# Optimization experiments

Hardware: AMD Instinct MI355X
Metric: run time of the kernel (lower is better)

## Reference

```python
import jax, jax.numpy as jnp
import numpy as np

VOL_SHAPE = (256, 256, 256)
DELTA = 1
EPS = 1e-8


def _radius_bins(shape, delta):
    # Frequency-index radius map (equivalent to distance from DC with fft wraparound),
    # binned into shells of width `delta`. Computed once with numpy (constant).
    axes = [np.fft.fftfreq(n) * n for n in shape]
    grids = np.meshgrid(*axes, indexing='ij')
    r = np.sqrt(sum(g.astype(np.float64) ** 2 for g in grids))
    bins = np.floor(r / delta).astype(np.int32)
    return bins.ravel(), int(bins.max()) + 1

_BINS, _NUM_SHELLS = _radius_bins(VOL_SHAPE, DELTA)
_BINS_J = jnp.asarray(_BINS)


def setup_inputs() -> dict:
    key = jax.random.key(0)
    kx, ky = jax.random.split(key)
    shp = (2, 1) + VOL_SHAPE
    X = jax.random.normal(kx, shp, dtype=jnp.float32)
    Y = jax.random.normal(ky, shp, dtype=jnp.float32)
    return {"X": X, "Y": Y}


def _fsc(X, Y):
    B, C = X.shape[0], X.shape[1]
    Fx = jnp.fft.fftn(X, axes=(-3, -2, -1))  # complex64 [B,C,D,H,W]
    Fy = jnp.fft.fftn(Y, axes=(-3, -2, -1))
    N = VOL_SHAPE[0] * VOL_SHAPE[1] * VOL_SHAPE[2]
    # Per-voxel quantities, flattened over the volume: [B*C, N]
    num = (Fx.real * Fy.real + Fx.imag * Fy.imag).reshape(B * C, N)  # Re(Fx * conj(Fy))
    px = (Fx.real ** 2 + Fx.imag ** 2).reshape(B * C, N)
    py = (Fy.real ** 2 + Fy.imag ** 2).reshape(B * C, N)
    seg = lambda v: jax.ops.segment_sum(v, _BINS_J, num_segments=_NUM_SHELLS)
    num_s = jax.vmap(seg)(num)  # [B*C, S]
    px_s = jax.vmap(seg)(px)
    py_s = jax.vmap(seg)(py)
    fsc = num_s / jnp.sqrt(px_s * py_s + EPS)  # [B*C, S]
    return fsc.reshape(B, C, _NUM_SHELLS)


def reference(X, Y):
    fsc = _fsc(X, Y)
    # size_average=True: average over radii, channel and batch -> scalar
    return jnp.mean(fsc)
```

## Files before the change

kernel.cpp:

```cpp
#include <hip/hip_runtime.h>
#include <math.h>

#define VOL (256 * 256 * 256)
#define NSHELL 222
#define SBINS 224
#define PI_D 3.14159265358979323846
#define VSTRIDE ((size_t)129 << 16)

__device__ __forceinline__ int rev4(int e) {
  return ((e & 3) << 6) | (((e >> 2) & 3) << 4) | (((e >> 4) & 3) << 2) | ((e >> 6) & 3);
}

__global__ void tw_init(float2* __restrict__ gtw) {
  int t = threadIdx.x;
  double a = -2.0 * PI_D * (double)t / 256.0;
  gtw[t] = make_float2((float)cos(a), (float)sin(a));
}

__device__ __forceinline__ void bfly4_dif(float* re, float* im, const float* twr,
                                          const float* twi, int a0, int a1, int a2,
                                          int a3, int t1, int t2, int t3) {
  float x0r = re[a0], x0i = im[a0], x1r = re[a1], x1i = im[a1];
  float x2r = re[a2], x2i = im[a2], x3r = re[a3], x3i = im[a3];
  float s02r = x0r + x2r, s02i = x0i + x2i, d02r = x0r - x2r, d02i = x0i - x2i;
  float s13r = x1r + x3r, s13i = x1i + x3i, d13r = x1r - x3r, d13i = x1i - x3i;
  re[a0] = s02r + s13r; im[a0] = s02i + s13i;
  float c1r = d02r + d13i, c1i = d02i - d13r;
  re[a1] = c1r * twr[t1] - c1i * twi[t1]; im[a1] = c1r * twi[t1] + c1i * twr[t1];
  float c2r = s02r - s13r, c2i = s02i - s13i;
  re[a2] = c2r * twr[t2] - c2i * twi[t2]; im[a2] = c2r * twi[t2] + c2i * twr[t2];
  float c3r = d02r - d13i, c3i = d02i + d13r;
  re[a3] = c3r * twr[t3] - c3i * twi[t3]; im[a3] = c3r * twi[t3] + c3i * twr[t3];
}

__device__ __forceinline__ void seg_flush(float* sh, int sb, float nv, float pv,
                                          float qv, int l) {
#pragma unroll
  for (int d = 1; d < 64; d <<= 1) {
    int sbo = __shfl_down(sb, d);
    float no = __shfl_down(nv, d);
    float po = __shfl_down(pv, d);
    float qo = __shfl_down(qv, d);
    if (l + d < 64 && sbo == sb) { nv += no; pv += po; qv += qo; }
  }
  int sbp = __shfl_up(sb, 1);
  if (l == 0 || sbp != sb) {
    atomicAdd(&sh[3 * sb + 0], nv);
    atomicAdd(&sh[3 * sb + 1], pv);
    atomicAdd(&sh[3 * sb + 2], qv);
  }
}

__global__ __launch_bounds__(256) void fft_z_pack(const float* __restrict__ X,
                                                  const float* __restrict__ Y,
                                                  float2* __restrict__ Gx,
                                                  float2* __restrict__ Gy,
                                                  const float2* __restrict__ gtw) {
  __shared__ float zr[256 * 17], zi[256 * 17];
  __shared__ float twr[256], twi[256];
  int t = threadIdx.x;
  { float2 w = gtw[t]; twr[t] = w.x; twi[t] = w.y; }
  int li = t >> 4, c = t & 15;
  int y = blockIdx.x >> 4;
  int x0 = (blockIdx.x & 15) << 4;
  const float4* xp = (const float4*)(X + (((size_t)(x0 + li)) << 16) + ((size_t)y << 8));
  const float4* yp = (const float4*)(Y + (((size_t)(x0 + li)) << 16) + ((size_t)y << 8));
#pragma unroll
  for (int it = 0; it < 4; ++it) {
    int e4 = c + 16 * it;
    float4 a = xp[e4];
    float4 b = yp[e4];
    int e = e4 << 2;
    zr[(e + 0) * 17 + li] = a.x; zi[(e + 0) * 17 + li] = b.x;
    zr[(e + 1) * 17 + li] = a.y; zi[(e + 1) * 17 + li] = b.y;
    zr[(e + 2) * 17 + li] = a.z; zi[(e + 2) * 17 + li] = b.z;
    zr[(e + 3) * 17 + li] = a.w; zi[(e + 3) * 17 + li] = b.w;
  }
  __syncthreads();
#pragma unroll
  for (int s = 0; s < 4; ++s) {
    int M = 64 >> (2 * s);
    int F = 1 << (2 * s);
#pragma unroll
    for (int ib = 0; ib < 4; ++ib) {
      int j = c + 16 * ib;
      int p = j & (M - 1);
      int jb = j >> (6 - 2 * s);
      int base = jb * (M << 2) + p;
      bfly4_dif(zr, zi, twr, twi, base * 17 + li, (base + M) * 17 + li,
                (base + 2 * M) * 17 + li, (base + 3 * M) * 17 + li,
                (p * F) & 255, (2 * p * F) & 255, (3 * p * F) & 255);
    }
    __syncthreads();
  }
  int krow = t >> 4, xi = t & 15;
#pragma unroll
  for (int g = 0; g < 9; ++g) {
    int kz = g * 16 + krow;
    if (kz <= 128) {
      int s1 = rev4(kz & 255);
      int s2 = rev4((256 - kz) & 255);
      float ar = zr[s1 * 17 + xi], ai = zi[s1 * 17 + xi];
      float br = zr[s2 * 17 + xi], bi = zi[s2 * 17 + xi];
      size_t off = ((size_t)kz << 16) + ((size_t)y << 8) + (size_t)(x0 + xi);
      Gx[off] = make_float2(0.5f * (ar + br), 0.5f * (ai - bi));
      Gy[off] = make_float2(0.5f * (ai + bi), 0.5f * (br - ar));
    }
  }
}

__global__ __launch_bounds__(256) void fft_y(float2* __restrict__ G,
                                             const float2* __restrict__ gtw) {
  __shared__ float sr[256 * 17], si[256 * 17];
  __shared__ float twr[256], twi[256];
  int t = threadIdx.x;
  { float2 w = gtw[t]; twr[t] = w.x; twi[t] = w.y; }
  int xi = t & 15, c = t >> 4;
  int x0 = blockIdx.x << 4;
  int kz = blockIdx.y;
  float2* Gp = G + (size_t)blockIdx.z * VSTRIDE + ((size_t)kz << 16) + (size_t)(x0 + xi);
#pragma unroll
  for (int i = 0; i < 16; ++i) {
    int e = c * 16 + i;
    float2 v = Gp[(size_t)e << 8];
    sr[e * 17 + xi] = v.x;
    si[e * 17 + xi] = v.y;
  }
  __syncthreads();
#pragma unroll
  for (int s = 0; s < 4; ++s) {
    int M = 64 >> (2 * s);
    int F = 1 << (2 * s);
#pragma unroll
    for (int ib = 0; ib < 4; ++ib) {
      int j = c + 16 * ib;
      int p = j & (M - 1);
      int jb = j >> (6 - 2 * s);
      int base = jb * (M << 2) + p;
      bfly4_dif(sr, si, twr, twi, base * 17 + xi, (base + M) * 17 + xi,
                (base + 2 * M) * 17 + xi, (base + 3 * M) * 17 + xi,
                (p * F) & 255, (2 * p * F) & 255, (3 * p * F) & 255);
    }
    __syncthreads();
  }
#pragma unroll
  for (int i = 0; i < 16; ++i) {
    int e = c * 16 + i;
    Gp[(size_t)e << 8] = make_float2(sr[e * 17 + xi], si[e * 17 + xi]);
  }
}

__global__ __launch_bounds__(512) void fft_x_reduce(const float2* __restrict__ G,
                                                    double* __restrict__ sums,
                                                    const float2* __restrict__ gtw) {
  __shared__ float Axr[256 * 9], Axi[256 * 9], Ayr[256 * 9], Ayi[256 * 9];
  __shared__ float twr[256], twi[256];
  __shared__ float sh[3 * SBINS];
  int t = threadIdx.x;
  if (t < 256) { float2 w = gtw[t]; twr[t] = w.x; twi[t] = w.y; }
  for (int i = t; i < 3 * SBINS; i += 512) sh[i] = 0.f;
  int vol = t >> 8, tt = t & 255;
  int li = tt >> 5, c = tt & 31;
  int kz = blockIdx.y;
  int r0 = blockIdx.x << 3;
  const float2* Gp = G + (size_t)vol * VSTRIDE + ((size_t)kz << 16) + ((size_t)(r0 + li) << 8);
  float* pr = vol ? Ayr : Axr;
  float* pi = vol ? Ayi : Axi;
#pragma unroll
  for (int it = 0; it < 8; ++it) {
    int e = c + 32 * it;
    float2 v = Gp[e];
    pr[e * 9 + li] = v.x;
    pi[e * 9 + li] = v.y;
  }
  __syncthreads();
#pragma unroll
  for (int s = 0; s < 3; ++s) {
    int M = 64 >> (2 * s);
    int F = 1 << (2 * s);
#pragma unroll
    for (int ib = 0; ib < 2; ++ib) {
      int j = c + 32 * ib;
      int p = j & (M - 1);
      int jb = j >> (6 - 2 * s);
      int base = jb * (M << 2) + p;
      bfly4_dif(pr, pi, twr, twi, base * 9 + li, (base + M) * 9 + li,
                (base + 2 * M) * 9 + li, (base + 3 * M) * 9 + li,
                (p * F) & 255, (2 * p * F) & 255, (3 * p * F) & 255);
    }
    __syncthreads();
  }
  float or_[2][4], oi_[2][4];
#pragma unroll
  for (int ib = 0; ib < 2; ++ib) {
    int j = c + 32 * ib;
    int base = 4 * j;
    float x0r = pr[(base + 0) * 9 + li], x0i = pi[(base + 0) * 9 + li];
    float x1r = pr[(base + 1) * 9 + li], x1i = pi[(base + 1) * 9 + li];
    float x2r = pr[(base + 2) * 9 + li], x2i = pi[(base + 2) * 9 + li];
    float x3r = pr[(base + 3) * 9 + li], x3i = pi[(base + 3) * 9 + li];
    float s02r = x0r + x2r, s02i = x0i + x2i, d02r = x0r - x2r, d02i = x0i - x2i;
    float s13r = x1r + x3r, s13i = x1i + x3i, d13r = x1r - x3r, d13i = x1i - x3i;
    or_[ib][0] = s02r + s13r; oi_[ib][0] = s02i + s13i;
    or_[ib][1] = d02r + d13i; oi_[ib][1] = d02i - d13r;
    or_[ib][2] = s02r - s13r; oi_[ib][2] = s02i - s13i;
    or_[ib][3] = d02r - d13i; oi_[ib][3] = d02i + d13r;
  }
  __syncthreads();
#pragma unroll
  for (int ib = 0; ib < 2; ++ib) {
    int j = c + 32 * ib;
#pragma unroll
    for (int q = 0; q < 4; ++q) {
      int slot = (q << 6) | ((j & 3) << 4) | (((j >> 2) & 3) << 2) | (j >> 4);
      pr[slot * 9 + li] = or_[ib][q];
      pi[slot * 9 + li] = oi_[ib][q];
    }
  }
  __syncthreads();
  int fz = kz - ((kz & 128) ? 256 : 0);
  int fz2 = fz * fz;
  {
    int w = t >> 6, l = t & 63;
    int ky = rev4(r0 + w);
    int fy = ky - ((ky & 128) ? 256 : 0);
    int c2 = fy * fy + fz2;
#pragma unroll
    for (int pass = 0; pass < 2; ++pass) {
      int kx = pass * 64 + l;
      int a = kx * 9 + w;
      float xr = Axr[a], xi = Axi[a], yr = Ayr[a], yi = Ayi[a];
      float nv = xr * yr + xi * yi;
      float pv = xr * xr + xi * xi;
      float qv = yr * yr + yi * yi;
      if (kx != 0) {
        int ma = ((256 - kx) & 255) * 9 + w;
        float mxr = Axr[ma], mxi = Axi[ma], myr = Ayr[ma], myi = Ayi[ma];
        nv += mxr * myr + mxi * myi;
        pv += mxr * mxr + mxi * mxi;
        qv += myr * myr + myi * myi;
      }
      int m = kx * kx + c2;
      int sb = (int)sqrtf((float)m);
      while (sb * sb > m) --sb;
      while ((sb + 1) * (sb + 1) <= m) ++sb;
      seg_flush(sh, sb, nv, pv, qv, l);
    }
    if (l == 0) {
      int a = 128 * 9 + w;
      float xr = Axr[a], xi = Axi[a], yr = Ayr[a], yi = Ayi[a];
      int m = 16384 + c2;
      int sb = (int)sqrtf((float)m);
      while (sb * sb > m) --sb;
      while ((sb + 1) * (sb + 1) <= m) ++sb;
      atomicAdd(&sh[3 * sb + 0], xr * yr + xi * yi);
      atomicAdd(&sh[3 * sb + 1], xr * xr + xi * xi);
      atomicAdd(&sh[3 * sb + 2], yr * yr + yi * yi);
    }
  }
  __syncthreads();
  float wf = (kz == 0 || kz == 128) ? 1.f : 2.f;
  for (int i = t; i < 3 * SBINS; i += 512) {
    float vv = sh[i];
    if (vv != 0.f) atomicAdd(&sums[i], (double)(wf * vv));
  }
}

__global__ void finalize(const double* __restrict__ sums, float* __restrict__ out) {
  if (threadIdx.x == 0 && blockIdx.x == 0) {
    double acc = 0.0;
    for (int b = 0; b < 2; ++b) {
      const double* s = sums + b * 3 * SBINS;
      for (int k = 0; k < NSHELL; ++k)
        acc += s[3 * k] / sqrt(s[3 * k + 1] * s[3 * k + 2] + 1e-8);
    }
    out[0] = (float)(acc / (2.0 * (double)NSHELL));
  }
}

extern "C" void kernel_launch(void* const* d_in, const int* in_sizes, int n_in,
                              void* d_out, int out_size, void* d_ws, size_t ws_size,
                              hipStream_t stream) {
  const float* X = (const float*)d_in[0];
  const float* Y = (const float*)d_in[1];
  float2* Gx = (float2*)d_ws;
  float2* Gy = Gx + VSTRIDE;
  double* sums = (double*)((char*)d_ws + (size_t)2 * VSTRIDE * sizeof(float2));
  float2* gtw = (float2*)(sums + 2 * 3 * SBINS);

  hipMemsetAsync(sums, 0, 2 * 3 * SBINS * sizeof(double), stream);
  tw_init<<<1, 256, 0, stream>>>(gtw);

  for (int b = 0; b < 2; ++b) {
    fft_z_pack<<<4096, 256, 0, stream>>>(X + (size_t)b * VOL, Y + (size_t)b * VOL, Gx, Gy, gtw);
    fft_y<<<dim3(16, 129, 2), 256, 0, stream>>>(Gx, gtw);
    fft_x_reduce<<<dim3(32, 129), 512, 0, stream>>>(Gx, sums + b * 3 * SBINS, gtw);
  }
  finalize<<<1, 1, 0, stream>>>(sums, (float*)d_out);
}
```

Measured before the change: 715.6 us.

## Use register-resident 16x16 FFTs for y/x passes and split global atomic accumulators

Replaces the shared-memory radix-4 stage loops in the y and x FFT kernels with a register-based 16x16 decomposition. Each thread does a 16-point FFT in registers, applies twiddles, makes one shared transpose, then does a second 16-point FFT. This cuts shared-memory traffic and barriers, and the x kernel now runs with 256 threads and natural output ordering. Global double atomics are spread across 16 partial-sum copies that a parallel finalize reduces, which lowers atomic contention at the cost of higher register pressure.

```diff
diff --git a/kernel.cpp b/kernel.cpp
--- a/kernel.cpp
+++ b/kernel.cpp
@@ -4,6 +4,7 @@
 #define VOL (256 * 256 * 256)
 #define NSHELL 222
 #define SBINS 224
+#define NSPLIT 16
 #define PI_D 3.14159265358979323846
 #define VSTRIDE ((size_t)129 << 16)
 
@@ -51,6 +52,50 @@
   }
 }
 
+__device__ __forceinline__ float2 cmul(float2 a, float2 b) {
+  return make_float2(a.x * b.x - a.y * b.y, a.x * b.y + a.y * b.x);
+}
+
+__device__ __forceinline__ void fft16(float2* v) {
+  const float C1 = 0.92387953251128674f;
+  const float S1 = 0.38268343236508978f;
+  const float R2 = 0.70710678118654752f;
+  float2 s[16];
+#pragma unroll
+  for (int p = 0; p < 4; ++p) {
+    float2 a = v[p], b = v[p + 4], cc = v[p + 8], d = v[p + 12];
+    float2 t0 = make_float2(a.x + cc.x, a.y + cc.y);
+    float2 t2 = make_float2(a.x - cc.x, a.y - cc.y);
+    float2 t1 = make_float2(b.x + d.x, b.y + d.y);
+    float2 t3 = make_float2(b.x - d.x, b.y - d.y);
+    s[p]      = make_float2(t0.x + t1.x, t0.y + t1.y);
+    s[p + 4]  = make_float2(t2.x + t3.y, t2.y - t3.x);
+    s[p + 8]  = make_float2(t0.x - t1.x, t0.y - t1.y);
+    s[p + 12] = make_float2(t2.x - t3.y, t2.y + t3.x);
+  }
+  s[5]  = cmul(s[5],  make_float2(C1, -S1));
+  s[6]  = cmul(s[6],  make_float2(R2, -R2));
+  s[7]  = cmul(s[7],  make_float2(S1, -C1));
+  s[9]  = cmul(s[9],  make_float2(R2, -R2));
+  s[10] = cmul(s[10], make_float2(0.f, -1.f));
+  s[11] = cmul(s[11], make_float2(-R2, -R2));
+  s[13] = cmul(s[13], make_float2(S1, -C1));
+  s[14] = cmul(s[14], make_float2(-R2, -R2));
+  s[15] = cmul(s[15], make_float2(-C1, S1));
+#pragma unroll
+  for (int r = 0; r < 4; ++r) {
+    float2 u0 = s[4 * r], u1 = s[4 * r + 1], u2 = s[4 * r + 2], u3 = s[4 * r + 3];
+    float2 e0 = make_float2(u0.x + u2.x, u0.y + u2.y);
+    float2 e1 = make_float2(u0.x - u2.x, u0.y - u2.y);
+    float2 o0 = make_float2(u1.x + u3.x, u1.y + u3.y);
+    float2 o1 = make_float2(u1.x - u3.x, u1.y - u3.y);
+    v[r]      = make_float2(e0.x + o0.x, e0.y + o0.y);
+    v[4 + r]  = make_float2(e1.x + o1.y, e1.y - o1.x);
+    v[8 + r]  = make_float2(e0.x - o0.x, e0.y - o0.y);
+    v[12 + r] = make_float2(e1.x - o1.y, e1.y + o1.x);
+  }
+}
+
 __global__ __launch_bounds__(256) void fft_z_pack(const float* __restrict__ X,
                                                   const float* __restrict__ Y,
                                                   float2* __restrict__ Gx,
@@ -109,136 +154,94 @@
   }
 }
 
-__global__ __launch_bounds__(256) void fft_y(float2* __restrict__ G,
-                                             const float2* __restrict__ gtw) {
-  __shared__ float sr[256 * 17], si[256 * 17];
-  __shared__ float twr[256], twi[256];
-  int t = threadIdx.x;
-  { float2 w = gtw[t]; twr[t] = w.x; twi[t] = w.y; }
-  int xi = t & 15, c = t >> 4;
+__global__ __launch_bounds__(256, 4) void fft_y(float2* __restrict__ G,
+                                                const float2* __restrict__ gtw) {
+  __shared__ float2 scr[16 * 273];
+  int t = threadIdx.x;
+  int xi = t & 15, h = t >> 4;
   int x0 = blockIdx.x << 4;
   int kz = blockIdx.y;
   float2* Gp = G + (size_t)blockIdx.z * VSTRIDE + ((size_t)kz << 16) + (size_t)(x0 + xi);
-#pragma unroll
-  for (int i = 0; i < 16; ++i) {
-    int e = c * 16 + i;
-    float2 v = Gp[(size_t)e << 8];
-    sr[e * 17 + xi] = v.x;
-    si[e * 17 + xi] = v.y;
-  }
-  __syncthreads();
-#pragma unroll
-  for (int s = 0; s < 4; ++s) {
-    int M = 64 >> (2 * s);
-    int F = 1 << (2 * s);
-#pragma unroll
-    for (int ib = 0; ib < 4; ++ib) {
-      int j = c + 16 * ib;
-      int p = j & (M - 1);
-      int jb = j >> (6 - 2 * s);
-      int base = jb * (M << 2) + p;
-      bfly4_dif(sr, si, twr, twi, base * 17 + xi, (base + M) * 17 + xi,
-                (base + 2 * M) * 17 + xi, (base + 3 * M) * 17 + xi,
-                (p * F) & 255, (2 * p * F) & 255, (3 * p * F) & 255);
-    }
-    __syncthreads();
-  }
-#pragma unroll
-  for (int i = 0; i < 16; ++i) {
-    int e = c * 16 + i;
-    Gp[(size_t)e << 8] = make_float2(sr[e * 17 + xi], si[e * 17 + xi]);
-  }
-}
-
-__global__ __launch_bounds__(512) void fft_x_reduce(const float2* __restrict__ G,
-                                                    double* __restrict__ sums,
-                                                    const float2* __restrict__ gtw) {
-  __shared__ float Axr[256 * 9], Axi[256 * 9], Ayr[256 * 9], Ayi[256 * 9];
-  __shared__ float twr[256], twi[256];
+  float2 v[16];
+#pragma unroll
+  for (int m = 0; m < 16; ++m) v[m] = Gp[(size_t)((m << 4) | h) << 8];
+  fft16(v);
+#pragma unroll
+  for (int k1 = 1; k1 < 16; ++k1) v[k1] = cmul(v[k1], gtw[h * k1]);
+  int wb = xi * 273 + h * 17;
+#pragma unroll
+  for (int k1 = 0; k1 < 16; ++k1) scr[wb + k1] = v[k1];
+  __syncthreads();
+  float2 u[16];
+  int rb = xi * 273 + h;
+#pragma unroll
+  for (int j2 = 0; j2 < 16; ++j2) u[j2] = scr[rb + j2 * 17];
+  fft16(u);
+#pragma unroll
+  for (int k2 = 0; k2 < 16; ++k2) Gp[(size_t)((k2 << 4) | h) << 8] = u[k2];
+}
+
+__global__ __launch_bounds__(256, 4) void fft_x_reduce(const float2* __restrict__ G,
+                                                       double* __restrict__ sums,
+                                                       const float2* __restrict__ gtw) {
+  __shared__ float2 pool[4672];
   __shared__ float sh[3 * SBINS];
   int t = threadIdx.x;
-  if (t < 256) { float2 w = gtw[t]; twr[t] = w.x; twi[t] = w.y; }
-  for (int i = t; i < 3 * SBINS; i += 512) sh[i] = 0.f;
-  int vol = t >> 8, tt = t & 255;
-  int li = tt >> 5, c = tt & 31;
+  for (int i = t; i < 3 * SBINS; i += 256) sh[i] = 0.f;
+  int vol = t >> 7, tt = t & 127;
+  int g = tt >> 4, c = tt & 15;
   int kz = blockIdx.y;
   int r0 = blockIdx.x << 3;
-  const float2* Gp = G + (size_t)vol * VSTRIDE + ((size_t)kz << 16) + ((size_t)(r0 + li) << 8);
-  float* pr = vol ? Ayr : Axr;
-  float* pi = vol ? Ayi : Axi;
-#pragma unroll
-  for (int it = 0; it < 8; ++it) {
-    int e = c + 32 * it;
-    float2 v = Gp[e];
-    pr[e * 9 + li] = v.x;
-    pi[e * 9 + li] = v.y;
-  }
-  __syncthreads();
-#pragma unroll
-  for (int s = 0; s < 3; ++s) {
-    int M = 64 >> (2 * s);
-    int F = 1 << (2 * s);
-#pragma unroll
-    for (int ib = 0; ib < 2; ++ib) {
-      int j = c + 32 * ib;
-      int p = j & (M - 1);
-      int jb = j >> (6 - 2 * s);
-      int base = jb * (M << 2) + p;
-      bfly4_dif(pr, pi, twr, twi, base * 9 + li, (base + M) * 9 + li,
-                (base + 2 * M) * 9 + li, (base + 3 * M) * 9 + li,
-                (p * F) & 255, (2 * p * F) & 255, (3 * p * F) & 255);
-    }
+  const float2* Gp = G + (size_t)vol * VSTRIDE + ((size_t)kz << 16) + ((size_t)(r0 + g) << 8);
+  float2 v[16];
+#pragma unroll
+  for (int m = 0; m < 16; ++m) v[m] = Gp[(m << 4) | c];
+  fft16(v);
+#pragma unroll
+  for (int k1 = 1; k1 < 16; ++k1) v[k1] = cmul(v[k1], gtw[c * k1]);
+  {
+    int sbase = ((vol << 3) | g) * 280;
+#pragma unroll
+    for (int k1 = 0; k1 < 16; ++k1) pool[sbase + c * 17 + k1] = v[k1];
+    float2 u[16];
+#pragma unroll
+    for (int j2 = 0; j2 < 16; ++j2) u[j2] = pool[sbase + j2 * 17 + c];
+    fft16(u);
     __syncthreads();
-  }
-  float or_[2][4], oi_[2][4];
-#pragma unroll
-  for (int ib = 0; ib < 2; ++ib) {
-    int j = c + 32 * ib;
-    int base = 4 * j;
-    float x0r = pr[(base + 0) * 9 + li], x0i = pi[(base + 0) * 9 + li];
-    float x1r = pr[(base + 1) * 9 + li], x1i = pi[(base + 1) * 9 + li];
-    float x2r = pr[(base + 2) * 9 + li], x2i = pi[(base + 2) * 9 + li];
-    float x3r = pr[(base + 3) * 9 + li], x3i = pi[(base + 3) * 9 + li];
-    float s02r = x0r + x2r, s02i = x0i + x2i, d02r = x0r - x2r, d02i = x0i - x2i;
-    float s13r = x1r + x3r, s13i = x1i + x3i, d13r = x1r - x3r, d13i = x1i - x3i;
-    or_[ib][0] = s02r + s13r; oi_[ib][0] = s02i + s13i;
-    or_[ib][1] = d02r + d13i; oi_[ib][1] = d02i - d13r;
-    or_[ib][2] = s02r - s13r; oi_[ib][2] = s02i - s13i;
-    or_[ib][3] = d02r - d13i; oi_[ib][3] = d02i + d13r;
-  }
-  __syncthreads();
-#pragma unroll
-  for (int ib = 0; ib < 2; ++ib) {
-    int j = c + 32 * ib;
-#pragma unroll
-    for (int q = 0; q < 4; ++q) {
-      int slot = (q << 6) | ((j & 3) << 4) | (((j >> 2) & 3) << 2) | (j >> 4);
-      pr[slot * 9 + li] = or_[ib][q];
-      pi[slot * 9 + li] = oi_[ib][q];
+    float2* A = pool + vol * 2336;
+#pragma unroll
+    for (int k2 = 0; k2 < 16; ++k2) {
+      int kx = (k2 << 4) | c;
+      A[kx * 9 + k2 + g] = u[k2];
     }
   }
   __syncthreads();
   int fz = kz - ((kz & 128) ? 256 : 0);
   int fz2 = fz * fz;
-  {
-    int w = t >> 6, l = t & 63;
-    int ky = rev4(r0 + w);
+  int w = t >> 6, l = t & 63;
+  const float2* Ax = pool;
+  const float2* Ay = pool + 2336;
+#pragma unroll
+  for (int rr = 0; rr < 2; ++rr) {
+    int row = (w << 1) | rr;
+    int ky = r0 + row;
     int fy = ky - ((ky & 128) ? 256 : 0);
     int c2 = fy * fy + fz2;
 #pragma unroll
     for (int pass = 0; pass < 2; ++pass) {
-      int kx = pass * 64 + l;
-      int a = kx * 9 + w;
-      float xr = Axr[a], xi = Axi[a], yr = Ayr[a], yi = Ayi[a];
-      float nv = xr * yr + xi * yi;
-      float pv = xr * xr + xi * xi;
-      float qv = yr * yr + yi * yi;
+      int kx = (pass << 6) | l;
+      float2 xv = Ax[kx * 9 + (kx >> 4) + row];
+      float2 yv = Ay[kx * 9 + (kx >> 4) + row];
+      float nv = xv.x * yv.x + xv.y * yv.y;
+      float pv = xv.x * xv.x + xv.y * xv.y;
+      float qv = yv.x * yv.x + yv.y * yv.y;
       if (kx != 0) {
-        int ma = ((256 - kx) & 255) * 9 + w;
-        float mxr = Axr[ma], mxi = Axi[ma], myr = Ayr[ma], myi = Ayi[ma];
-        nv += mxr * myr + mxi * myi;
-        pv += mxr * mxr + mxi * mxi;
-        qv += myr * myr + myi * myi;
+        int mk = 256 - kx;
+        float2 mx = Ax[mk * 9 + (mk >> 4) + row];
+        float2 my = Ay[mk * 9 + (mk >> 4) + row];
+        nv += mx.x * my.x + mx.y * my.y;
+        pv += mx.x * mx.x + mx.y * mx.y;
+        qv += my.x * my.x + my.y * my.y;
       }
       int m = kx * kx + c2;
       int sb = (int)sqrtf((float)m);
@@ -247,30 +250,42 @@
       seg_flush(sh, sb, nv, pv, qv, l);
     }
     if (l == 0) {
-      int a = 128 * 9 + w;
-      float xr = Axr[a], xi = Axi[a], yr = Ayr[a], yi = Ayi[a];
+      float2 xv = Ax[128 * 9 + 8 + row];
+      float2 yv = Ay[128 * 9 + 8 + row];
       int m = 16384 + c2;
       int sb = (int)sqrtf((float)m);
       while (sb * sb > m) --sb;
       while ((sb + 1) * (sb + 1) <= m) ++sb;
-      atomicAdd(&sh[3 * sb + 0], xr * yr + xi * yi);
-      atomicAdd(&sh[3 * sb + 1], xr * xr + xi * xi);
-      atomicAdd(&sh[3 * sb + 2], yr * yr + yi * yi);
+      atomicAdd(&sh[3 * sb + 0], xv.x * yv.x + xv.y * yv.y);
+      atomicAdd(&sh[3 * sb + 1], xv.x * xv.x + xv.y * xv.y);
+      atomicAdd(&sh[3 * sb + 2], yv.x * yv.x + yv.y * yv.y);
     }
   }
   __syncthreads();
   float wf = (kz == 0 || kz == 128) ? 1.f : 2.f;
-  for (int i = t; i < 3 * SBINS; i += 512) {
+  double* sp = sums + (size_t)(blockIdx.x & (NSPLIT - 1)) * (3 * SBINS);
+  for (int i = t; i < 3 * SBINS; i += 256) {
     float vv = sh[i];
-    if (vv != 0.f) atomicAdd(&sums[i], (double)(wf * vv));
+    if (vv != 0.f) atomicAdd(&sp[i], (double)(wf * vv));
   }
 }
 
 __global__ void finalize(const double* __restrict__ sums, float* __restrict__ out) {
-  if (threadIdx.x == 0 && blockIdx.x == 0) {
+  __shared__ double red[2 * 3 * SBINS];
+  int t = threadIdx.x;
+  for (int i = t; i < 2 * 3 * SBINS; i += 256) {
+    int b = i / (3 * SBINS), k = i - b * (3 * SBINS);
+    const double* s = sums + (size_t)b * NSPLIT * 3 * SBINS + k;
+    double a = 0.0;
+#pragma unroll
+    for (int sp = 0; sp < NSPLIT; ++sp) a += s[(size_t)sp * 3 * SBINS];
+    red[i] = a;
+  }
+  __syncthreads();
+  if (t == 0) {
     double acc = 0.0;
     for (int b = 0; b < 2; ++b) {
-      const double* s = sums + b * 3 * SBINS;
+      const double* s = red + b * 3 * SBINS;
       for (int k = 0; k < NSHELL; ++k)
         acc += s[3 * k] / sqrt(s[3 * k + 1] * s[3 * k + 2] + 1e-8);
     }
@@ -286,15 +301,15 @@
   float2* Gx = (float2*)d_ws;
   float2* Gy = Gx + VSTRIDE;
   double* sums = (double*)((char*)d_ws + (size_t)2 * VSTRIDE * sizeof(float2));
-  float2* gtw = (float2*)(sums + 2 * 3 * SBINS);
-
-  hipMemsetAsync(sums, 0, 2 * 3 * SBINS * sizeof(double), stream);
+  float2* gtw = (float2*)(sums + (size_t)2 * NSPLIT * 3 * SBINS);
+
+  hipMemsetAsync(sums, 0, (size_t)2 * NSPLIT * 3 * SBINS * sizeof(double), stream);
   tw_init<<<1, 256, 0, stream>>>(gtw);
 
   for (int b = 0; b < 2; ++b) {
     fft_z_pack<<<4096, 256, 0, stream>>>(X + (size_t)b * VOL, Y + (size_t)b * VOL, Gx, Gy, gtw);
     fft_y<<<dim3(16, 129, 2), 256, 0, stream>>>(Gx, gtw);
-    fft_x_reduce<<<dim3(32, 129), 512, 0, stream>>>(Gx, sums + b * 3 * SBINS, gtw);
-  }
-  finalize<<<1, 1, 0, stream>>>(sums, (float*)d_out);
-}
+    fft_x_reduce<<<dim3(32, 129), 256, 0, stream>>>(Gx, sums + (size_t)b * NSPLIT * 3 * SBINS, gtw);
+  }
+  finalize<<<1, 256, 0, stream>>>(sums, (float*)d_out);
+}
```

Result: faster. 611.1 us (-14.6%).
